# Kernel tuning notes

Hardware: AMD Instinct MI355X
Metric: run time of the kernel (lower is better)

The kernel has to match this reference:

```python
import jax, jax.numpy as jnp
import numpy as np

WH, WW = 7, 7          # window size
SH, SW = 3, 3          # shift size
NUM_HEADS = 8


def setup_inputs() -> dict:
    key = jax.random.key(0)
    ks = jax.random.split(key, 5)
    B, H, W, C = 32, 56, 56, 256
    return {
        "x": jax.random.normal(ks[0], (B, H * W, C), dtype=jnp.float32),
        "w_qkv": jax.random.normal(ks[1], (C, 3 * C), dtype=jnp.float32) * (C ** -0.5),
        "b_qkv": jax.random.normal(ks[2], (3 * C,), dtype=jnp.float32) * 0.02,
        "w_proj": jax.random.normal(ks[3], (C, C), dtype=jnp.float32) * (C ** -0.5),
        "b_proj": jax.random.normal(ks[4], (C,), dtype=jnp.float32) * 0.02,
        "H": H,
        "W": W,
    }


def reference(x, w_qkv, b_qkv, w_proj, b_proj, H, W):
    B, N, C = x.shape
    nh = NUM_HEADS
    hd = C // nh
    nwh, nww = H // WH, W // WW

    xi = x.reshape(B, H, W, C)
    if SH > 0 or SW > 0:
        xi = jnp.roll(xi, shift=(-SH, -SW), axis=(1, 2))
    # window partition: [B*nwh*nww, WH*WW, C]
    xw = xi.reshape(B, nwh, WH, nww, WW, C).transpose(0, 1, 3, 2, 4, 5)
    xw = xw.reshape(-1, WH * WW, C)

    qkv = xw @ w_qkv + b_qkv                     # [nW, 49, 3C]
    qkv = qkv.reshape(-1, WH * WW, 3, nh, hd).transpose(2, 0, 3, 1, 4)
    q, k, v = qkv[0], qkv[1], qkv[2]             # each [nW, nh, 49, hd]

    attn = jnp.einsum('whqd,whkd->whqk', q, k) * (hd ** -0.5)
    attn = jax.nn.softmax(attn, axis=-1)
    out = jnp.einsum('whqk,whkd->whqd', attn, v)  # [nW, nh, 49, hd]
    out = out.transpose(0, 2, 1, 3).reshape(-1, WH * WW, C)
    out = out @ w_proj + b_proj

    # window merge
    out = out.reshape(B, nwh, nww, WH, WW, C).transpose(0, 1, 3, 2, 4, 5)
    out = out.reshape(B, H, W, C)
    if SH > 0 or SW > 0:
        out = jnp.roll(out, shift=(SH, SW), axis=(1, 2))
    return out.reshape(B, N, C)
```

## Files before the change

### kernel.cpp

```cpp
#include <hip/hip_runtime.h>
#include <hip/hip_bf16.h>

typedef __attribute__((ext_vector_type(8))) short bf16x8;
typedef __attribute__((ext_vector_type(4))) float f32x4;

#define MFMA32(A,B,C) __builtin_amdgcn_mfma_f32_16x16x32_bf16(A,B,C,0,0,0)

__device__ __forceinline__ short f2bf(float f) {
    union { float f; unsigned u; } v; v.f = f;
    unsigned r = v.u + 0x7FFFu + ((v.u >> 16) & 1u);
    return (short)(r >> 16);
}

__global__ void prep_weights(const float* __restrict__ wqkv,
                             const float* __restrict__ wproj,
                             short* __restrict__ wqkvT,
                             short* __restrict__ wprojT) {
    const int n = blockIdx.x, k = threadIdx.x;
    if (n < 768) wqkvT[n * 256 + k] = f2bf(wqkv[k * 768 + n]);
    else         wprojT[(n - 768) * 256 + k] = f2bf(wproj[k * 256 + (n - 768)]);
}

#define QK_PASS(WPTR, BOFF, SCALE, FOUT)                                                   \
  {                                                                                        \
    f32x4 acc[2][4];                                                                       \
    _Pragma("unroll") for (int h=0;h<2;++h)                                                \
      _Pragma("unroll") for (int t=0;t<4;++t) acc[h][t]=(f32x4){0.f,0.f,0.f,0.f};          \
    _Pragma("unroll") for (int kk=0;kk<8;++kk) {                                           \
      bf16x8 xf[4];                                                                        \
      _Pragma("unroll") for (int t=0;t<4;++t) {                                            \
        const int row = t*16 + l15;                                                        \
        xf[t] = *(const bf16x8*)(smem + row*512 + (((kk<<6)+(l4<<4)) ^ ((row&7)<<4)));     \
      }                                                                                    \
      _Pragma("unroll") for (int h=0;h<2;++h) {                                            \
        bf16x8 wf = *(const bf16x8*)((WPTR) + (h*16+l15)*256 + (kk<<5) + (l4<<3));         \
        _Pragma("unroll") for (int t=0;t<4;++t)                                            \
          acc[h][t] = MFMA32(wf, xf[t], acc[h][t]);                                        \
      }                                                                                    \
    }                                                                                      \
    _Pragma("unroll") for (int h=0;h<2;++h) {                                              \
      f32x4 bias = *(const f32x4*)(bqkv + (BOFF) + h*16 + (l4<<2));                        \
      _Pragma("unroll") for (int t=0;t<4;++t)                                               \
        _Pragma("unroll") for (int rg=0;rg<4;++rg)                                         \
          FOUT[t][h*4+rg] = f2bf((acc[h][t][rg] + bias[rg]) * (SCALE));                    \
    }                                                                                      \
  }

__launch_bounds__(512, 2)
__global__ void winattn_fused(const float* __restrict__ x,
                              const float* __restrict__ bqkv,
                              const float* __restrict__ bproj,
                              const short* __restrict__ wqkvT,
                              const short* __restrict__ wprojT,
                              float* __restrict__ out) {
    __shared__ char smem[65536];
    char* cbuf = smem + 32768;
    const int tid = threadIdx.x;
    const int wid = blockIdx.x;
    const int b  = wid >> 6;
    const int wh = (wid >> 3) & 7;
    const int ww = wid & 7;

    {
        const int r  = tid >> 3;
        const int cb = (tid & 7) << 5;
        if (r < 49) {
            const int i = r / 7, j = r - i * 7;
            int h  = wh * 7 + i + 3; if (h  >= 56) h  -= 56;
            int wc = ww * 7 + j + 3; if (wc >= 56) wc -= 56;
            const float* src = x + (((size_t)(b * 56 + h)) * 56 + wc) * 256 + cb;
            #pragma unroll
            for (int c = 0; c < 4; ++c) {
                f32x4 f0 = *(const f32x4*)(src + c * 8);
                f32x4 f1 = *(const f32x4*)(src + c * 8 + 4);
                bf16x8 o;
                #pragma unroll
                for (int q = 0; q < 4; ++q) { o[q] = f2bf(f0[q]); o[q + 4] = f2bf(f1[q]); }
                const int colbyte = (cb + c * 8) * 2;
                *(bf16x8*)(smem + r * 512 + (colbyte ^ ((r & 7) << 4))) = o;
            }
        } else {
            bf16x8 z;
            #pragma unroll
            for (int q = 0; q < 8; ++q) z[q] = 0;
            #pragma unroll
            for (int c = 0; c < 4; ++c) {
                const int colbyte = (cb + c * 8) * 2;
                *(bf16x8*)(smem + r * 512 + (colbyte ^ ((r & 7) << 4))) = z;
            }
        }
    }
    __syncthreads();

    const int wv  = tid >> 6;
    const int l   = tid & 63;
    const int l15 = l & 15;
    const int l4  = l >> 4;

    const short* wq  = wqkvT + ((wv << 5) << 8);
    const short* wk  = wq + (256 << 8);
    const short* wvv = wq + (512 << 8);

    bf16x8 qp[4], kp[4];
    QK_PASS(wq, (wv << 5), 0.17677669529663687f, qp)
    QK_PASS(wk, 256 + (wv << 5), 1.0f, kp)

    bf16x8 pp[4][2];
    #pragma unroll
    for (int qt = 0; qt < 4; ++qt) {
        f32x4 sQ[4];
        #pragma unroll
        for (int t = 0; t < 4; ++t) sQ[t] = (f32x4){0.f, 0.f, 0.f, 0.f};
        #pragma unroll
        for (int t = 0; t < 4; ++t)
            sQ[t] = MFMA32(kp[t], qp[qt], sQ[t]);

        float m = -1e30f;
        #pragma unroll
        for (int t = 0; t < 4; ++t)
            #pragma unroll
            for (int rg = 0; rg < 4; ++rg) {
                const bool valid = (t < 3) || ((l4 | rg) == 0);
                float v0 = valid ? sQ[t][rg] : -1e30f;
                sQ[t][rg] = v0;
                m = fmaxf(m, v0);
            }
        m = fmaxf(m, __shfl_xor(m, 16));
        m = fmaxf(m, __shfl_xor(m, 32));
        float s = 0.f;
        #pragma unroll
        for (int t = 0; t < 4; ++t)
            #pragma unroll
            for (int rg = 0; rg < 4; ++rg) {
                float e = __expf(sQ[t][rg] - m);
                sQ[t][rg] = e;
                s += e;
            }
        s += __shfl_xor(s, 16);
        s += __shfl_xor(s, 32);
        const float inv = 1.f / s;
        #pragma unroll
        for (int t = 0; t < 4; ++t)
            #pragma unroll
            for (int rg = 0; rg < 4; ++rg)
                pp[qt][t >> 1][(t & 1) * 4 + rg] = f2bf(sQ[t][rg] * inv);
    }

    bf16x8 vp[2][2];
    {
        f32x4 acc[4][2];
        #pragma unroll
        for (int t = 0; t < 4; ++t)
            #pragma unroll
            for (int h = 0; h < 2; ++h) acc[t][h] = (f32x4){0.f, 0.f, 0.f, 0.f};
        #pragma unroll
        for (int kk = 0; kk < 8; ++kk) {
            bf16x8 xf[4];
            #pragma unroll
            for (int t = 0; t < 4; ++t) {
                const int row = t * 16 + l15;
                xf[t] = *(const bf16x8*)(smem + row * 512 + (((kk << 6) + (l4 << 4)) ^ ((row & 7) << 4)));
            }
            #pragma unroll
            for (int h = 0; h < 2; ++h) {
                bf16x8 wf = *(const bf16x8*)(wvv + (h * 16 + l15) * 256 + (kk << 5) + (l4 << 3));
                #pragma unroll
                for (int t = 0; t < 4; ++t)
                    acc[t][h] = MFMA32(xf[t], wf, acc[t][h]);
            }
        }
        #pragma unroll
        for (int h = 0; h < 2; ++h) {
            const float bias = bqkv[512 + (wv << 5) + h * 16 + l15];
            #pragma unroll
            for (int t = 0; t < 4; ++t)
                #pragma unroll
                for (int rg = 0; rg < 4; ++rg)
                    vp[t >> 1][h][(t & 1) * 4 + rg] = f2bf(acc[t][h][rg] + bias);
        }
    }

    f32x4 o[4][2];
    #pragma unroll
    for (int qt = 0; qt < 4; ++qt)
        #pragma unroll
        for (int h = 0; h < 2; ++h) o[qt][h] = (f32x4){0.f, 0.f, 0.f, 0.f};
    #pragma unroll
    for (int tp = 0; tp < 2; ++tp)
        #pragma unroll
        for (int h = 0; h < 2; ++h)
            #pragma unroll
            for (int qt = 0; qt < 4; ++qt)
                o[qt][h] = MFMA32(pp[qt][tp], vp[tp][h], o[qt][h]);

    #pragma unroll
    for (int qt = 0; qt < 4; ++qt)
        #pragma unroll
        for (int h = 0; h < 2; ++h)
            #pragma unroll
            for (int rg = 0; rg < 4; ++rg) {
                const int row = qt * 16 + (l4 << 2) + rg;
                const int col = (wv << 5) + (h << 4) + l15;
                *(short*)(cbuf + row * 512 + ((col * 2) ^ ((row & 7) << 4))) = f2bf(o[qt][h][rg]);
            }
    __syncthreads();

    f32x4 po[2][4];
    #pragma unroll
    for (int c = 0; c < 2; ++c)
        #pragma unroll
        for (int r = 0; r < 4; ++r) po[c][r] = (f32x4){0.f, 0.f, 0.f, 0.f};

    #pragma unroll
    for (int kk = 0; kk < 8; ++kk) {
        bf16x8 a[4];
        #pragma unroll
        for (int rt = 0; rt < 4; ++rt) {
            const int row = rt * 16 + l15;
            a[rt] = *(const bf16x8*)(cbuf + row * 512 + (((kk << 6) + (l4 << 4)) ^ ((row & 7) << 4)));
        }
        #pragma unroll
        for (int ct = 0; ct < 2; ++ct) {
            const short* bp = wprojT + (((wv << 5) + (ct << 4) + l15) << 8) + (kk << 5) + (l4 << 3);
            bf16x8 bfr = *(const bf16x8*)bp;
            #pragma unroll
            for (int rt = 0; rt < 4; ++rt)
                po[ct][rt] = MFMA32(a[rt], bfr, po[ct][rt]);
        }
    }

    #pragma unroll
    for (int ct = 0; ct < 2; ++ct) {
        const int col = (wv << 5) + (ct << 4) + l15;
        const float bias = bproj[col];
        #pragma unroll
        for (int rt = 0; rt < 4; ++rt) {
            #pragma unroll
            for (int rg = 0; rg < 4; ++rg) {
                const int row = rt * 16 + (l4 << 2) + rg;
                if (row < 49) {
                    const int i = row / 7, j = row - i * 7;
                    int h  = wh * 7 + i + 3; if (h  >= 56) h  -= 56;
                    int wc = ww * 7 + j + 3; if (wc >= 56) wc -= 56;
                    out[(((size_t)(b * 56 + h)) * 56 + wc) * 256 + col] = po[ct][rt][rg] + bias;
                }
            }
        }
    }
}

extern "C" void kernel_launch(void* const* d_in, const int* in_sizes, int n_in,
                              void* d_out, int out_size, void* d_ws, size_t ws_size,
                              hipStream_t stream) {
    const float* x     = (const float*)d_in[0];
    const float* wqkv  = (const float*)d_in[1];
    const float* bqkv  = (const float*)d_in[2];
    const float* wproj = (const float*)d_in[3];
    const float* bproj = (const float*)d_in[4];
    float* out = (float*)d_out;

    short* wqkvT  = (short*)d_ws;
    short* wprojT = wqkvT + 768 * 256;

    prep_weights<<<dim3(1024), dim3(256), 0, stream>>>(wqkv, wproj, wqkvT, wprojT);
    winattn_fused<<<dim3(2048), dim3(512), 0, stream>>>(x, bqkv, bproj, wqkvT, wprojT, out);
}
```

Baseline: 189.7 us.

## Reuse input LDS buffer for attention output and compute PV per query tile

Computes V before softmax, then adds a barrier so the x tile in shared memory can be overwritten by the attention output. This halves shared memory from 64KB to 32KB per block. The PV product is now done per query tile, with operands swapped so the output is transposed, and written as packed 4-element bf16 stores instead of scalar shorts. Keeping fewer probability registers live lowers register pressure. Together these aim to raise occupancy and cut LDS store count, at the cost of an extra block-wide barrier.

```diff
diff --git a/kernel.cpp b/kernel.cpp
--- a/kernel.cpp
+++ b/kernel.cpp
@@ -1,6 +1,7 @@
 #include <hip/hip_runtime.h>
 #include <hip/hip_bf16.h>
 
+typedef __attribute__((ext_vector_type(4))) short bf16x4;
 typedef __attribute__((ext_vector_type(8))) short bf16x8;
 typedef __attribute__((ext_vector_type(4))) float f32x4;
 
@@ -40,7 +41,7 @@
     }                                                                                      \
     _Pragma("unroll") for (int h=0;h<2;++h) {                                              \
       f32x4 bias = *(const f32x4*)(bqkv + (BOFF) + h*16 + (l4<<2));                        \
-      _Pragma("unroll") for (int t=0;t<4;++t)                                               \
+      _Pragma("unroll") for (int t=0;t<4;++t)                                              \
         _Pragma("unroll") for (int rg=0;rg<4;++rg)                                         \
           FOUT[t][h*4+rg] = f2bf((acc[h][t][rg] + bias[rg]) * (SCALE));                    \
     }                                                                                      \
@@ -53,8 +54,7 @@
                               const short* __restrict__ wqkvT,
                               const short* __restrict__ wprojT,
                               float* __restrict__ out) {
-    __shared__ char smem[65536];
-    char* cbuf = smem + 32768;
+    __shared__ char smem[32768];
     const int tid = threadIdx.x;
     const int wid = blockIdx.x;
     const int b  = wid >> 6;
@@ -105,7 +105,41 @@
     QK_PASS(wq, (wv << 5), 0.17677669529663687f, qp)
     QK_PASS(wk, 256 + (wv << 5), 1.0f, kp)
 
-    bf16x8 pp[4][2];
+    bf16x8 vp[2][2];
+    {
+        f32x4 acc[4][2];
+        #pragma unroll
+        for (int t = 0; t < 4; ++t)
+            #pragma unroll
+            for (int h = 0; h < 2; ++h) acc[t][h] = (f32x4){0.f, 0.f, 0.f, 0.f};
+        #pragma unroll
+        for (int kk = 0; kk < 8; ++kk) {
+            bf16x8 xf[4];
+            #pragma unroll
+            for (int t = 0; t < 4; ++t) {
+                const int row = t * 16 + l15;
+                xf[t] = *(const bf16x8*)(smem + row * 512 + (((kk << 6) + (l4 << 4)) ^ ((row & 7) << 4)));
+            }
+            #pragma unroll
+            for (int h = 0; h < 2; ++h) {
+                bf16x8 wf = *(const bf16x8*)(wvv + (h * 16 + l15) * 256 + (kk << 5) + (l4 << 3));
+                #pragma unroll
+                for (int t = 0; t < 4; ++t)
+                    acc[t][h] = MFMA32(xf[t], wf, acc[t][h]);
+            }
+        }
+        #pragma unroll
+        for (int h = 0; h < 2; ++h) {
+            const float bias = bqkv[512 + (wv << 5) + h * 16 + l15];
+            #pragma unroll
+            for (int t = 0; t < 4; ++t)
+                #pragma unroll
+                for (int rg = 0; rg < 4; ++rg)
+                    vp[t >> 1][h][(t & 1) * 4 + rg] = f2bf(acc[t][h][rg] + bias);
+        }
+    }
+    __syncthreads();
+
     #pragma unroll
     for (int qt = 0; qt < 4; ++qt) {
         f32x4 sQ[4];
@@ -139,70 +173,27 @@
         s += __shfl_xor(s, 16);
         s += __shfl_xor(s, 32);
         const float inv = 1.f / s;
+
+        bf16x8 pf[2];
         #pragma unroll
         for (int t = 0; t < 4; ++t)
             #pragma unroll
             for (int rg = 0; rg < 4; ++rg)
-                pp[qt][t >> 1][(t & 1) * 4 + rg] = f2bf(sQ[t][rg] * inv);
-    }
-
-    bf16x8 vp[2][2];
-    {
-        f32x4 acc[4][2];
-        #pragma unroll
-        for (int t = 0; t < 4; ++t)
-            #pragma unroll
-            for (int h = 0; h < 2; ++h) acc[t][h] = (f32x4){0.f, 0.f, 0.f, 0.f};
-        #pragma unroll
-        for (int kk = 0; kk < 8; ++kk) {
-            bf16x8 xf[4];
-            #pragma unroll
-            for (int t = 0; t < 4; ++t) {
-                const int row = t * 16 + l15;
-                xf[t] = *(const bf16x8*)(smem + row * 512 + (((kk << 6) + (l4 << 4)) ^ ((row & 7) << 4)));
-            }
-            #pragma unroll
-            for (int h = 0; h < 2; ++h) {
-                bf16x8 wf = *(const bf16x8*)(wvv + (h * 16 + l15) * 256 + (kk << 5) + (l4 << 3));
-                #pragma unroll
-                for (int t = 0; t < 4; ++t)
-                    acc[t][h] = MFMA32(xf[t], wf, acc[t][h]);
-            }
-        }
+                pf[t >> 1][(t & 1) * 4 + rg] = f2bf(sQ[t][rg] * inv);
+
         #pragma unroll
         for (int h = 0; h < 2; ++h) {
-            const float bias = bqkv[512 + (wv << 5) + h * 16 + l15];
-            #pragma unroll
-            for (int t = 0; t < 4; ++t)
-                #pragma unroll
-                for (int rg = 0; rg < 4; ++rg)
-                    vp[t >> 1][h][(t & 1) * 4 + rg] = f2bf(acc[t][h][rg] + bias);
-        }
-    }
-
-    f32x4 o[4][2];
-    #pragma unroll
-    for (int qt = 0; qt < 4; ++qt)
-        #pragma unroll
-        for (int h = 0; h < 2; ++h) o[qt][h] = (f32x4){0.f, 0.f, 0.f, 0.f};
-    #pragma unroll
-    for (int tp = 0; tp < 2; ++tp)
-        #pragma unroll
-        for (int h = 0; h < 2; ++h)
-            #pragma unroll
-            for (int qt = 0; qt < 4; ++qt)
-                o[qt][h] = MFMA32(pp[qt][tp], vp[tp][h], o[qt][h]);
-
-    #pragma unroll
-    for (int qt = 0; qt < 4; ++qt)
-        #pragma unroll
-        for (int h = 0; h < 2; ++h)
-            #pragma unroll
-            for (int rg = 0; rg < 4; ++rg) {
-                const int row = qt * 16 + (l4 << 2) + rg;
-                const int col = (wv << 5) + (h << 4) + l15;
-                *(short*)(cbuf + row * 512 + ((col * 2) ^ ((row & 7) << 4))) = f2bf(o[qt][h][rg]);
-            }
+            f32x4 oq = (f32x4){0.f, 0.f, 0.f, 0.f};
+            oq = MFMA32(vp[0][h], pf[0], oq);
+            oq = MFMA32(vp[1][h], pf[1], oq);
+            bf16x4 ob;
+            #pragma unroll
+            for (int rg = 0; rg < 4; ++rg) ob[rg] = f2bf(oq[rg]);
+            const int row = qt * 16 + l15;
+            const int colbyte = ((wv << 5) + (h << 4) + (l4 << 2)) * 2;
+            *(bf16x4*)(smem + row * 512 + (colbyte ^ ((row & 7) << 4))) = ob;
+        }
+    }
     __syncthreads();
 
     f32x4 po[2][4];
@@ -217,7 +208,7 @@
         #pragma unroll
         for (int rt = 0; rt < 4; ++rt) {
             const int row = rt * 16 + l15;
-            a[rt] = *(const bf16x8*)(cbuf + row * 512 + (((kk << 6) + (l4 << 4)) ^ ((row & 7) << 4)));
+            a[rt] = *(const bf16x8*)(smem + row * 512 + (((kk << 6) + (l4 << 4)) ^ ((row & 7) << 4)));
         }
         #pragma unroll
         for (int ct = 0; ct < 2; ++ct) {
```

Result: no change. 192.4 us (+1.4%).
